# Optimization experiments

Hardware: AMD Instinct MI355X
Metric: run time of the kernel (lower is better)

Reference implementation:

```python
import jax, jax.numpy as jnp
import numpy as np

N, F, F1 = 8192, 256, 64
EDGE_PROB = 0.01  # adjacency density


def setup_inputs() -> dict:
    key = jax.random.key(0)
    kX, kA, kW, ka = jax.random.split(key, 4)
    X = jax.random.normal(kX, (N, F), dtype=jnp.float32)
    # binary adjacency mask (float, as in the original where A multiplies the -1e10 mask)
    A = (jax.random.uniform(kA, (N, N)) < EDGE_PROB).astype(jnp.float32)
    # glorot_uniform init for W [F1, F] and a [2, F1, 1]
    limW = float(np.sqrt(6.0 / (F1 + F)))
    W = jax.random.uniform(kW, (F1, F), minval=-limW, maxval=limW, dtype=jnp.float32)
    lima = float(np.sqrt(6.0 / (F1 + 1)))
    a = jax.random.uniform(ka, (2, F1, 1), minval=-lima, maxval=lima, dtype=jnp.float32)
    return {"X": X, "A": A, "W": W, "a": a}


def reference(X, A, W, a):
    x_features = X @ W.T                       # [N, F1]
    att_self = x_features @ a[0]               # [N, 1]
    att_neighbours = x_features @ a[1]         # [N, 1]
    att = att_self + att_neighbours.T          # [N, N] broadcast additive score
    att = jnp.where(att > 0, att, 0.2 * att)   # LeakyReLU(alpha=0.2)
    att_masked = att + (-1e10) * (1.0 - A)     # mask non-edges
    dense = jax.nn.softmax(att_masked, axis=0) # column-wise softmax (axis=0, as in source)
    return dense @ x_features                  # [N, F1]
```

## Files before the change

### kernel.cpp

```cpp
#include <hip/hip_runtime.h>
#include <math.h>

#define NN   8192
#define FF   256
#define FF1  64
#define CAP  256

__global__ __launch_bounds__(256) void k1_feat(const float* __restrict__ X,
                                               const float* __restrict__ W,
                                               const float* __restrict__ a,
                                               float* __restrict__ xf,
                                               float* __restrict__ s,
                                               float* __restrict__ t,
                                               float* __restrict__ D) {
    __shared__ float Xs[32 * FF];
    const int tid  = threadIdx.x;
    const int row0 = blockIdx.x * 32;

    {
        const int gid = blockIdx.x * 256 + tid;
        if (gid < NN / 4) ((float4*)D)[gid] = make_float4(0.f, 0.f, 0.f, 0.f);
    }

    const float4* Xg  = (const float4*)(X + (size_t)row0 * FF);
    float4*       Xs4 = (float4*)Xs;
#pragma unroll
    for (int v = 0; v < 8; ++v) Xs4[tid + v * 256] = Xg[tid + v * 256];
    __syncthreads();

    const int f  = tid & 63;
    const int rg = tid >> 6;

    float acc[8] = {0.f,0.f,0.f,0.f,0.f,0.f,0.f,0.f};
    const float4* Wrow = (const float4*)(W + (size_t)f * FF);
    for (int k4 = 0; k4 < FF / 4; ++k4) {
        float4 wv = Wrow[k4];
#pragma unroll
        for (int r = 0; r < 8; ++r) {
            float4 xv = *(const float4*)&Xs[(rg * 8 + r) * FF + k4 * 4];
            acc[r] = fmaf(wv.x, xv.x, acc[r]);
            acc[r] = fmaf(wv.y, xv.y, acc[r]);
            acc[r] = fmaf(wv.z, xv.z, acc[r]);
            acc[r] = fmaf(wv.w, xv.w, acc[r]);
        }
    }

    const float a0 = a[f];
    const float a1 = a[FF1 + f];
#pragma unroll
    for (int r = 0; r < 8; ++r) {
        const int row = row0 + rg * 8 + r;
        xf[(size_t)row * FF1 + f] = acc[r];
        float vs = acc[r] * a0;
        float vt = acc[r] * a1;
#pragma unroll
        for (int off = 32; off; off >>= 1) {
            vs += __shfl_xor(vs, off);
            vt += __shfl_xor(vt, off);
        }
        if (f == 0) { s[row] = vs; t[row] = vt; }
    }
}

__global__ __launch_bounds__(256) void kScan(const float* __restrict__ A,
                                             const float* __restrict__ s,
                                             const float* __restrict__ t,
                                             unsigned short* __restrict__ idx,
                                             float* __restrict__ ev,
                                             float* __restrict__ D,
                                             int* __restrict__ counts) {
    const int tid  = threadIdx.x;
    const int lane = tid & 63;
    const int wv   = tid >> 6;
    __shared__ unsigned short lbuf[256 * 8];
    __shared__ int wtot[4];

    for (int r = 0; r < 4; ++r) {
        const int i = blockIdx.x * 4 + r;
        int c = 0;
        const float4* Arow = (const float4*)(A + (size_t)i * NN);
#pragma unroll
        for (int k = 0; k < 8; ++k) {
            const int v = tid + k * 256;
            float4 av = Arow[v];
            if (av.x != 0.f) { lbuf[tid * 8 + (c & 7)] = (unsigned short)(4 * v + 0); ++c; }
            if (av.y != 0.f) { lbuf[tid * 8 + (c & 7)] = (unsigned short)(4 * v + 1); ++c; }
            if (av.z != 0.f) { lbuf[tid * 8 + (c & 7)] = (unsigned short)(4 * v + 2); ++c; }
            if (av.w != 0.f) { lbuf[tid * 8 + (c & 7)] = (unsigned short)(4 * v + 3); ++c; }
        }
        if (c > 8) c = 8;

        int sc = c;
#pragma unroll
        for (int off = 1; off < 64; off <<= 1) {
            int n = __shfl_up(sc, off);
            if (lane >= off) sc += n;
        }
        if (lane == 63) wtot[wv] = sc;
        __syncthreads();

        int base = sc - c;
#pragma unroll
        for (int w = 0; w < 4; ++w) if (w < wv) base += wtot[w];

        const float si = s[i];
        for (int q = 0; q < c; ++q) {
            const int pos = base + q;
            if (pos < CAP) {
                const int j    = lbuf[tid * 8 + q];
                const float x  = si + t[j];
                const float lr = x > 0.f ? x : 0.2f * x;
                const float e  = __expf(lr);
                idx[(size_t)i * CAP + pos] = (unsigned short)j;
                ev [(size_t)i * CAP + pos] = e;
                unsafeAtomicAdd(&D[j], e);
            }
        }
        if (tid == 255) counts[i] = (base + c < CAP) ? (base + c) : CAP;
        __syncthreads();
    }
}

__global__ __launch_bounds__(256) void k3_apply(const float* __restrict__ xf,
                                                const float* __restrict__ D,
                                                const unsigned short* __restrict__ idx,
                                                const float* __restrict__ ev,
                                                const int* __restrict__ counts,
                                                float* __restrict__ out) {
    const int wave = threadIdx.x >> 6;
    const int lane = threadIdx.x & 63;
    const int i    = blockIdx.x * 4 + wave;

    const int cnt = counts[i];
    float acc0 = 0.f, acc1 = 0.f, acc2 = 0.f, acc3 = 0.f;

    for (int base = 0; base < cnt; base += 64) {
        const int p = base + lane;
        const bool act = (p < cnt);
        int   jj = act ? (int)idx[(size_t)i * CAP + p] : 0;
        float ww = act ? ev[(size_t)i * CAP + p] / D[jj] : 0.f;

#pragma unroll
        for (int e = 0; e < 64; e += 4) {
            { const int je = __builtin_amdgcn_readlane(jj, e + 0);
              const float we = __int_as_float(__builtin_amdgcn_readlane(__float_as_int(ww), e + 0));
              acc0 = fmaf(we, xf[(size_t)je * FF1 + lane], acc0); }
            { const int je = __builtin_amdgcn_readlane(jj, e + 1);
              const float we = __int_as_float(__builtin_amdgcn_readlane(__float_as_int(ww), e + 1));
              acc1 = fmaf(we, xf[(size_t)je * FF1 + lane], acc1); }
            { const int je = __builtin_amdgcn_readlane(jj, e + 2);
              const float we = __int_as_float(__builtin_amdgcn_readlane(__float_as_int(ww), e + 2));
              acc2 = fmaf(we, xf[(size_t)je * FF1 + lane], acc2); }
            { const int je = __builtin_amdgcn_readlane(jj, e + 3);
              const float we = __int_as_float(__builtin_amdgcn_readlane(__float_as_int(ww), e + 3));
              acc3 = fmaf(we, xf[(size_t)je * FF1 + lane], acc3); }
        }
    }
    out[(size_t)i * FF1 + lane] = (acc0 + acc1) + (acc2 + acc3);
}

extern "C" void kernel_launch(void* const* d_in, const int* in_sizes, int n_in,
                              void* d_out, int out_size, void* d_ws, size_t ws_size,
                              hipStream_t stream) {
    const float* X = (const float*)d_in[0];
    const float* A = (const float*)d_in[1];
    const float* W = (const float*)d_in[2];
    const float* a = (const float*)d_in[3];
    float* out = (float*)d_out;

    char* ws = (char*)d_ws;
    float* xf = (float*)ws;                                  ws += (size_t)NN * FF1 * 4;
    float* s  = (float*)ws;                                  ws += (size_t)NN * 4;
    float* t  = (float*)ws;                                  ws += (size_t)NN * 4;
    float* D  = (float*)ws;                                  ws += (size_t)NN * 4;
    int*   counts = (int*)ws;                                ws += (size_t)NN * 4;
    unsigned short* idx = (unsigned short*)ws;               ws += (size_t)NN * CAP * 2;
    float* ev = (float*)ws;

    k1_feat<<<NN / 32, 256, 0, stream>>>(X, W, a, xf, s, t, D);
    kScan  <<<NN / 4,  256, 0, stream>>>(A, s, t, idx, ev, D, counts);
    k3_apply<<<NN / 4, 256, 0, stream>>>(xf, D, idx, ev, counts, out);
}
```

Baseline: 96.46 us.

## Replace scan barriers with LDS atomics and shrink feature tiles for more blocks

In the adjacency scan kernel, the cross-wave prefix sum now uses a shared-memory atomicAdd per wave plus a global atomic for row counts, instead of two __syncthreads per row. This lets waves proceed independently. The feature kernel now processes 8 rows per block instead of 32, giving 4x more blocks and lower LDS use, and it zero-initialises counts. The trade-offs are a non-deterministic order of entries within each row and less reuse of W loads in the feature GEMM.

```diff
diff --git a/kernel.cpp b/kernel.cpp
--- a/kernel.cpp
+++ b/kernel.cpp
@@ -12,53 +12,54 @@
                                                float* __restrict__ xf,
                                                float* __restrict__ s,
                                                float* __restrict__ t,
-                                               float* __restrict__ D) {
-    __shared__ float Xs[32 * FF];
+                                               float* __restrict__ D,
+                                               int* __restrict__ counts) {
+    __shared__ float Xs[8 * FF];
     const int tid  = threadIdx.x;
-    const int row0 = blockIdx.x * 32;
+    const int lane = tid & 63;
+    const int wv   = tid >> 6;
+    const int row0 = blockIdx.x * 8;
 
     {
         const int gid = blockIdx.x * 256 + tid;
-        if (gid < NN / 4) ((float4*)D)[gid] = make_float4(0.f, 0.f, 0.f, 0.f);
+        if (gid < NN / 4) {
+            ((float4*)D)[gid]    = make_float4(0.f, 0.f, 0.f, 0.f);
+            ((int4*)counts)[gid] = make_int4(0, 0, 0, 0);
+        }
     }
 
     const float4* Xg  = (const float4*)(X + (size_t)row0 * FF);
     float4*       Xs4 = (float4*)Xs;
-#pragma unroll
-    for (int v = 0; v < 8; ++v) Xs4[tid + v * 256] = Xg[tid + v * 256];
+    Xs4[tid]       = Xg[tid];
+    Xs4[tid + 256] = Xg[tid + 256];
     __syncthreads();
 
-    const int f  = tid & 63;
-    const int rg = tid >> 6;
-
-    float acc[8] = {0.f,0.f,0.f,0.f,0.f,0.f,0.f,0.f};
+    const int f  = lane;
+    const int r0 = wv * 2;
+    float acc0 = 0.f, acc1 = 0.f;
     const float4* Wrow = (const float4*)(W + (size_t)f * FF);
     for (int k4 = 0; k4 < FF / 4; ++k4) {
-        float4 wv = Wrow[k4];
+        const float4 wq = Wrow[k4];
+        const float4 x0 = *(const float4*)&Xs[r0 * FF + k4 * 4];
+        const float4 x1 = *(const float4*)&Xs[(r0 + 1) * FF + k4 * 4];
+        acc0 = fmaf(wq.x, x0.x, acc0); acc0 = fmaf(wq.y, x0.y, acc0);
+        acc0 = fmaf(wq.z, x0.z, acc0); acc0 = fmaf(wq.w, x0.w, acc0);
+        acc1 = fmaf(wq.x, x1.x, acc1); acc1 = fmaf(wq.y, x1.y, acc1);
+        acc1 = fmaf(wq.z, x1.z, acc1); acc1 = fmaf(wq.w, x1.w, acc1);
+    }
+    const float a0 = a[f], a1 = a[FF1 + f];
+    xf[(size_t)(row0 + r0) * FF1 + f]     = acc0;
+    xf[(size_t)(row0 + r0 + 1) * FF1 + f] = acc1;
+    float vs0 = acc0 * a0, vt0 = acc0 * a1;
+    float vs1 = acc1 * a0, vt1 = acc1 * a1;
 #pragma unroll
-        for (int r = 0; r < 8; ++r) {
-            float4 xv = *(const float4*)&Xs[(rg * 8 + r) * FF + k4 * 4];
-            acc[r] = fmaf(wv.x, xv.x, acc[r]);
-            acc[r] = fmaf(wv.y, xv.y, acc[r]);
-            acc[r] = fmaf(wv.z, xv.z, acc[r]);
-            acc[r] = fmaf(wv.w, xv.w, acc[r]);
-        }
+    for (int off = 32; off; off >>= 1) {
+        vs0 += __shfl_xor(vs0, off); vt0 += __shfl_xor(vt0, off);
+        vs1 += __shfl_xor(vs1, off); vt1 += __shfl_xor(vt1, off);
     }
-
-    const float a0 = a[f];
-    const float a1 = a[FF1 + f];
-#pragma unroll
-    for (int r = 0; r < 8; ++r) {
-        const int row = row0 + rg * 8 + r;
-        xf[(size_t)row * FF1 + f] = acc[r];
-        float vs = acc[r] * a0;
-        float vt = acc[r] * a1;
-#pragma unroll
-        for (int off = 32; off; off >>= 1) {
-            vs += __shfl_xor(vs, off);
-            vt += __shfl_xor(vt, off);
-        }
-        if (f == 0) { s[row] = vs; t[row] = vt; }
+    if (lane == 0) {
+        s[row0 + r0] = vs0; s[row0 + r0 + 1] = vs1;
+        t[row0 + r0] = vt0; t[row0 + r0 + 1] = vt1;
     }
 }
 
@@ -71,9 +72,11 @@
                                              int* __restrict__ counts) {
     const int tid  = threadIdx.x;
     const int lane = tid & 63;
-    const int wv   = tid >> 6;
     __shared__ unsigned short lbuf[256 * 8];
-    __shared__ int wtot[4];
+    __shared__ int cnt4[4];
+
+    if (tid < 4) cnt4[tid] = 0;
+    __syncthreads();
 
     for (int r = 0; r < 4; ++r) {
         const int i = blockIdx.x * 4 + r;
@@ -96,12 +99,13 @@
             int n = __shfl_up(sc, off);
             if (lane >= off) sc += n;
         }
-        if (lane == 63) wtot[wv] = sc;
-        __syncthreads();
-
-        int base = sc - c;
-#pragma unroll
-        for (int w = 0; w < 4; ++w) if (w < wv) base += wtot[w];
+        int wbase = 0;
+        if (lane == 63) {
+            wbase = atomicAdd(&cnt4[r], sc);
+            atomicAdd(&counts[i], sc);
+        }
+        wbase = __shfl(wbase, 63);
+        const int base = wbase + sc - c;
 
         const float si = s[i];
         for (int q = 0; q < c; ++q) {
@@ -116,8 +120,6 @@
                 unsafeAtomicAdd(&D[j], e);
             }
         }
-        if (tid == 255) counts[i] = (base + c < CAP) ? (base + c) : CAP;
-        __syncthreads();
     }
 }
 
@@ -131,7 +133,8 @@
     const int lane = threadIdx.x & 63;
     const int i    = blockIdx.x * 4 + wave;
 
-    const int cnt = counts[i];
+    int cnt = counts[i];
+    if (cnt > CAP) cnt = CAP;
     float acc0 = 0.f, acc1 = 0.f, acc2 = 0.f, acc3 = 0.f;
 
     for (int base = 0; base < cnt; base += 64) {
@@ -177,7 +180,7 @@
     unsigned short* idx = (unsigned short*)ws;               ws += (size_t)NN * CAP * 2;
     float* ev = (float*)ws;
 
-    k1_feat<<<NN / 32, 256, 0, stream>>>(X, W, a, xf, s, t, D);
-    kScan  <<<NN / 4,  256, 0, stream>>>(A, s, t, idx, ev, D, counts);
+    k1_feat<<<NN / 8, 256, 0, stream>>>(X, W, a, xf, s, t, D, counts);
+    kScan  <<<NN / 4, 256, 0, stream>>>(A, s, t, idx, ev, D, counts);
     k3_apply<<<NN / 4, 256, 0, stream>>>(xf, D, idx, ev, counts, out);
 }
```

New measurement: 112.5 us. 16.6% more time.

## Split edge exp and atomics out of scan; recompute edge weights in apply

Applied to the files above, without the earlier changes.

The scan kernel now only compacts adjacency indices. A new kEdge kernel computes the exp scores and atomically accumulates the column sums, and the apply kernel recomputes exp(leakyrelu(s_i+t_j)) instead of reading a stored ev array. This drops the ev buffer writes and reads and takes the serialized per-thread exp and atomic loop out of the A-streaming scan. In exchange it adds a kernel launch and computes the exponential twice per edge.

```diff
diff --git a/kernel.cpp b/kernel.cpp
--- a/kernel.cpp
+++ b/kernel.cpp
@@ -63,11 +63,7 @@
 }
 
 __global__ __launch_bounds__(256) void kScan(const float* __restrict__ A,
-                                             const float* __restrict__ s,
-                                             const float* __restrict__ t,
                                              unsigned short* __restrict__ idx,
-                                             float* __restrict__ ev,
-                                             float* __restrict__ D,
                                              int* __restrict__ counts) {
     const int tid  = threadIdx.x;
     const int lane = tid & 63;
@@ -103,42 +99,60 @@
 #pragma unroll
         for (int w = 0; w < 4; ++w) if (w < wv) base += wtot[w];
 
-        const float si = s[i];
         for (int q = 0; q < c; ++q) {
             const int pos = base + q;
-            if (pos < CAP) {
-                const int j    = lbuf[tid * 8 + q];
-                const float x  = si + t[j];
-                const float lr = x > 0.f ? x : 0.2f * x;
-                const float e  = __expf(lr);
-                idx[(size_t)i * CAP + pos] = (unsigned short)j;
-                ev [(size_t)i * CAP + pos] = e;
-                unsafeAtomicAdd(&D[j], e);
-            }
+            if (pos < CAP) idx[(size_t)i * CAP + pos] = lbuf[tid * 8 + q];
         }
         if (tid == 255) counts[i] = (base + c < CAP) ? (base + c) : CAP;
         __syncthreads();
     }
 }
 
+__global__ __launch_bounds__(256) void kEdge(const float* __restrict__ s,
+                                             const float* __restrict__ t,
+                                             const unsigned short* __restrict__ idx,
+                                             const int* __restrict__ counts,
+                                             float* __restrict__ D) {
+    const int wv   = threadIdx.x >> 6;
+    const int lane = threadIdx.x & 63;
+    const int i    = blockIdx.x * 4 + wv;
+
+    const int   cnt = counts[i];
+    const float si  = s[i];
+    for (int p = lane; p < cnt; p += 64) {
+        const int j    = idx[(size_t)i * CAP + p];
+        const float x  = si + t[j];
+        const float lr = x > 0.f ? x : 0.2f * x;
+        unsafeAtomicAdd(&D[j], __expf(lr));
+    }
+}
+
 __global__ __launch_bounds__(256) void k3_apply(const float* __restrict__ xf,
+                                                const float* __restrict__ s,
+                                                const float* __restrict__ t,
                                                 const float* __restrict__ D,
                                                 const unsigned short* __restrict__ idx,
-                                                const float* __restrict__ ev,
                                                 const int* __restrict__ counts,
                                                 float* __restrict__ out) {
     const int wave = threadIdx.x >> 6;
     const int lane = threadIdx.x & 63;
     const int i    = blockIdx.x * 4 + wave;
 
-    const int cnt = counts[i];
+    const int   cnt = counts[i];
+    const float si  = s[i];
     float acc0 = 0.f, acc1 = 0.f, acc2 = 0.f, acc3 = 0.f;
 
     for (int base = 0; base < cnt; base += 64) {
         const int p = base + lane;
         const bool act = (p < cnt);
-        int   jj = act ? (int)idx[(size_t)i * CAP + p] : 0;
-        float ww = act ? ev[(size_t)i * CAP + p] / D[jj] : 0.f;
+        int   jj = 0;
+        float ww = 0.f;
+        if (act) {
+            jj = (int)idx[(size_t)i * CAP + p];
+            const float x  = si + t[jj];
+            const float lr = x > 0.f ? x : 0.2f * x;
+            ww = __expf(lr) / D[jj];
+        }
 
 #pragma unroll
         for (int e = 0; e < 64; e += 4) {
@@ -174,10 +188,10 @@
     float* t  = (float*)ws;                                  ws += (size_t)NN * 4;
     float* D  = (float*)ws;                                  ws += (size_t)NN * 4;
     int*   counts = (int*)ws;                                ws += (size_t)NN * 4;
-    unsigned short* idx = (unsigned short*)ws;               ws += (size_t)NN * CAP * 2;
-    float* ev = (float*)ws;
+    unsigned short* idx = (unsigned short*)ws;
 
     k1_feat<<<NN / 32, 256, 0, stream>>>(X, W, a, xf, s, t, D);
-    kScan  <<<NN / 4,  256, 0, stream>>>(A, s, t, idx, ev, D, counts);
-    k3_apply<<<NN / 4, 256, 0, stream>>>(xf, D, idx, ev, counts, out);
+    kScan  <<<NN / 4,  256, 0, stream>>>(A, idx, counts);
+    kEdge  <<<NN / 4,  256, 0, stream>>>(s, t, idx, counts, D);
+    k3_apply<<<NN / 4, 256, 0, stream>>>(xf, s, t, D, idx, counts, out);
 }
```

Result: slower. 127.7 us (+32.4%).
